# Performance work log

Hardware: AMD Instinct MI355X
Metric: run time of the kernel (lower is better)

Reference implementation:

```python
import jax, jax.numpy as jnp
import numpy as np

N_NODES = 50000
N_EDGES = 800000
SD = 128
N_GRAPHS = 128
HL = 4
VOCAB = 1340
N_CLASSES = 41
BN_EPS = 1e-5


def setup_inputs() -> dict:
    key = jax.random.key(0)
    ks = jax.random.split(key, 20)
    s = 1.0 / np.sqrt(SD)
    inp = {
        "node_ids": jax.random.randint(ks[0], (N_NODES,), 0, VOCAB),
        "edge_index": jax.random.randint(ks[1], (2, N_EDGES), 0, N_NODES),
        "batch": jnp.sort(jax.random.randint(ks[2], (N_NODES,), 0, N_GRAPHS)),
        "emb": jax.random.normal(ks[3], (VOCAB, SD)) * 0.05,
        "in_W1": jax.random.normal(ks[4], (SD, SD)) * s,
        "in_b1": jnp.zeros((SD,)),
        "in_W2": jax.random.normal(ks[5], (SD, SD)) * s,
        "in_b2": jnp.zeros((SD,)),
        "bn_gamma": jnp.ones((SD,)),
        "bn_beta": jnp.zeros((SD,)),
        "bn_mean": jnp.zeros((SD,)),
        "bn_var": jnp.ones((SD,)),
        "out_W1": jax.random.normal(ks[6], (SD, SD)) * s,
        "out_b1": jnp.zeros((SD,)),
        "out_W2": jax.random.normal(ks[7], (SD, SD)) * s,
        "out_b2": jnp.zeros((SD,)),
        "fc1_W": jax.random.normal(ks[8], (SD, SD)) * s,
        "fc1_b": jnp.zeros((SD,)),
        "fc2_W": jax.random.normal(ks[9], (N_CLASSES, SD)) * s,
        "fc2_b": jnp.zeros((N_CLASSES,)),
    }
    return inp


def reference(node_ids, edge_index, batch, emb, in_W1, in_b1, in_W2, in_b2,
              bn_gamma, bn_beta, bn_mean, bn_var,
              out_W1, out_b1, out_W2, out_b2, fc1_W, fc1_b, fc2_W, fc2_b):
    src, dst = edge_index[0], edge_index[1]

    def gin(x, W1, b1, W2, b2):
        # GINConv with eps=0: mlp(x + sum_{j in N(i)} x_j)
        agg = jax.ops.segment_sum(x[src], dst, num_segments=N_NODES)
        h = x + agg
        h = jnp.maximum(h @ W1.T + b1, 0.0)
        return h @ W2.T + b2

    def bn(x):
        # eval-mode BatchNorm1d with running stats
        return (x - bn_mean) * (bn_gamma / jnp.sqrt(bn_var + BN_EPS)) + bn_beta

    x = emb[node_ids]  # [N, SD]
    x = bn(jnp.maximum(gin(x, in_W1, in_b1, in_W2, in_b2), 0.0))
    for _ in range(HL):  # shared weights, repeated hl times
        x = bn(jnp.maximum(gin(x, in_W1, in_b1, in_W2, in_b2), 0.0))
    x = jnp.maximum(gin(x, out_W1, out_b1, out_W2, out_b2), 0.0)
    pooled = jax.ops.segment_sum(x, batch, num_segments=N_GRAPHS)  # [G, SD]
    h = jnp.maximum(pooled @ fc1_W.T + fc1_b, 0.0)
    return h @ fc2_W.T + fc2_b  # [G, 41]
```

## Files before the change

kernel.cpp:

```cpp
#include <hip/hip_runtime.h>

#define NN 50000
#define NE 800000
#define NG 128
#define NC 41
#define CAP 64
#define XG 8
#define RNG 6250

typedef __attribute__((ext_vector_type(8))) short bfrag8;
typedef __attribute__((ext_vector_type(4))) float facc4;

__device__ __forceinline__ float bf2f(unsigned short u) {
  union { unsigned int i; float f; } v; v.i = ((unsigned int)u) << 16; return v.f;
}
__device__ __forceinline__ unsigned short f2bf(float f) {
  union { float f; unsigned int i; } v; v.f = f;
  unsigned int x = v.i;
  x += 0x7fffu + ((x >> 16) & 1u);
  return (unsigned short)(x >> 16);
}
__device__ __forceinline__ void acc_u4(const uint4 u, float* a) {
  union { unsigned int i; float f; } c;
  c.i = u.x << 16;          a[0] += c.f;
  c.i = u.x & 0xffff0000u;  a[1] += c.f;
  c.i = u.y << 16;          a[2] += c.f;
  c.i = u.y & 0xffff0000u;  a[3] += c.f;
  c.i = u.z << 16;          a[4] += c.f;
  c.i = u.z & 0xffff0000u;  a[5] += c.f;
  c.i = u.w << 16;          a[6] += c.f;
  c.i = u.w & 0xffff0000u;  a[7] += c.f;
}
__device__ __forceinline__ unsigned int pack2(float lo, float hi) {
  return (unsigned int)f2bf(lo) | ((unsigned int)f2bf(hi) << 16);
}

__global__ void prep_kernel(const float* __restrict__ W1, const float* __restrict__ W2,
                            const float* __restrict__ oW1, const float* __restrict__ oW2,
                            const float* __restrict__ gamma, const float* __restrict__ beta,
                            const float* __restrict__ mean, const float* __restrict__ var,
                            unsigned short* W1b, unsigned short* W2b,
                            unsigned short* oW1b, unsigned short* oW2b,
                            float* scale, float* shift) {
  int i = blockIdx.x * 256 + threadIdx.x;
  if (i < 128 * 128) {
    W1b[i] = f2bf(W1[i]);
    W2b[i] = f2bf(W2[i]);
    oW1b[i] = f2bf(oW1[i]);
    oW2b[i] = f2bf(oW2[i]);
  }
  if (i < 128) {
    float s = gamma[i] * rsqrtf(var[i] + 1e-5f);
    scale[i] = s;
    shift[i] = beta[i] - mean[i] * s;
  }
}

__global__ void embed_kernel(const int* __restrict__ node_ids, const float* __restrict__ emb,
                             unsigned short* __restrict__ xb) {
  int idx = blockIdx.x * 256 + threadIdx.x;
  if (idx >= NN * 32) return;
  int node = idx >> 5, f = (idx & 31) * 4;
  const float4 v = *(const float4*)&emb[node_ids[node] * 128 + f];
  ushort4 o;
  o.x = f2bf(v.x); o.y = f2bf(v.y); o.z = f2bf(v.z); o.w = f2bf(v.w);
  *(ushort4*)&xb[node * 128 + f] = o;
}

__global__ __launch_bounds__(256) void fill_kernel(const int* __restrict__ ei,
                                                   int* __restrict__ cnt,
                                                   unsigned short* __restrict__ srclist) {
  int b = blockIdx.x;
  int g = b & 7;
  int s = b >> 3;
  int e = s * 256 + threadIdx.x;
  if (e >= NE) return;
  int d = ei[NE + e];
  unsigned int lo = g * RNG;
  if ((unsigned int)(d - lo) < (unsigned int)RNG) {
    int src = ei[e];
    int pos = atomicAdd(&cnt[d], 1);
    if (pos < CAP) srclist[d * CAP + pos] = (unsigned short)src;
  }
}

__global__ __launch_bounds__(256) void agg_kernel(const unsigned short* __restrict__ xb,
                                                  const int* __restrict__ cnt,
                                                  const unsigned short* __restrict__ srclist,
                                                  unsigned short* __restrict__ hb) {
  int tid = threadIdx.x;
  int node = blockIdx.x * 16 + (tid >> 4);
  if (node >= NN) return;
  int f = (tid & 15) * 8;
  float a[8];
  acc_u4(*(const uint4*)&xb[node * 128 + f],
         (a[0]=0.f, a[1]=0.f, a[2]=0.f, a[3]=0.f, a[4]=0.f, a[5]=0.f, a[6]=0.f, a[7]=0.f, a));
  int deg = cnt[node];
  if (deg > CAP) deg = CAP;
  const unsigned short* lst = &srclist[node * CAP];
  int j = 0;
  for (; j + 8 <= deg; j += 8) {
    uint4 u0 = *(const uint4*)&xb[(int)lst[j] * 128 + f];
    uint4 u1 = *(const uint4*)&xb[(int)lst[j + 1] * 128 + f];
    uint4 u2 = *(const uint4*)&xb[(int)lst[j + 2] * 128 + f];
    uint4 u3 = *(const uint4*)&xb[(int)lst[j + 3] * 128 + f];
    uint4 u4 = *(const uint4*)&xb[(int)lst[j + 4] * 128 + f];
    uint4 u5 = *(const uint4*)&xb[(int)lst[j + 5] * 128 + f];
    uint4 u6 = *(const uint4*)&xb[(int)lst[j + 6] * 128 + f];
    uint4 u7 = *(const uint4*)&xb[(int)lst[j + 7] * 128 + f];
    acc_u4(u0, a); acc_u4(u1, a); acc_u4(u2, a); acc_u4(u3, a);
    acc_u4(u4, a); acc_u4(u5, a); acc_u4(u6, a); acc_u4(u7, a);
  }
  for (; j + 4 <= deg; j += 4) {
    uint4 u0 = *(const uint4*)&xb[(int)lst[j] * 128 + f];
    uint4 u1 = *(const uint4*)&xb[(int)lst[j + 1] * 128 + f];
    uint4 u2 = *(const uint4*)&xb[(int)lst[j + 2] * 128 + f];
    uint4 u3 = *(const uint4*)&xb[(int)lst[j + 3] * 128 + f];
    acc_u4(u0, a); acc_u4(u1, a); acc_u4(u2, a); acc_u4(u3, a);
  }
  for (; j < deg; ++j) {
    uint4 u = *(const uint4*)&xb[(int)lst[j] * 128 + f];
    acc_u4(u, a);
  }
  uint4 o;
  o.x = pack2(a[0], a[1]); o.y = pack2(a[2], a[3]);
  o.z = pack2(a[4], a[5]); o.w = pack2(a[6], a[7]);
  *(uint4*)&hb[node * 128 + f] = o;
}

__global__ __launch_bounds__(256) void mlp_kernel(const unsigned short* __restrict__ A,
                                                  const unsigned short* __restrict__ W1b,
                                                  const unsigned short* __restrict__ W2b,
                                                  const float* __restrict__ bias1,
                                                  const float* __restrict__ bias2,
                                                  const float* __restrict__ scale,
                                                  const float* __restrict__ shift,
                                                  unsigned short* __restrict__ Out,
                                                  int M, int mode) {
  __shared__ unsigned short sW[128 * 128];
  __shared__ unsigned short sA[64 * 128];
  int tid = threadIdx.x;
  int bRow = blockIdx.x * 64;

  const uint4* gw1 = (const uint4*)W1b;
#pragma unroll
  for (int p = 0; p < 8; ++p) {
    int g = p * 256 + tid;
    int r = g >> 4, b = g & 15;
    int ph = (b + r) & 15;
    *(uint4*)&sW[(r * 16 + ph) * 8] = gw1[g];
  }
#pragma unroll
  for (int p = 0; p < 4; ++p) {
    int g = p * 256 + tid;
    int r = g >> 4, b = g & 15;
    int ph = (b + r) & 15;
    int grow = bRow + r;
    uint4 v = {0u, 0u, 0u, 0u};
    if (grow < M) v = *(const uint4*)&A[grow * 128 + b * 8];
    *(uint4*)&sA[(r * 16 + ph) * 8] = v;
  }
  __syncthreads();

  int wave = tid >> 6;
  int lane = tid & 63;
  int l16 = lane & 15;
  int quad = lane >> 4;
  int arow = wave * 16 + l16;

  {
    bfrag8 af[4];
#pragma unroll
    for (int k = 0; k < 4; ++k) {
      int ph = (k * 4 + quad + arow) & 15;
      af[k] = *(const bfrag8*)&sA[(arow * 16 + ph) * 8];
    }
    facc4 acc[8];
#pragma unroll
    for (int t = 0; t < 8; ++t) acc[t] = (facc4){0.f, 0.f, 0.f, 0.f};
#pragma unroll
    for (int k = 0; k < 4; ++k) {
#pragma unroll
      for (int t = 0; t < 8; ++t) {
        int r = t * 16 + l16;
        int ph = (k * 4 + quad + r) & 15;
        bfrag8 bf = *(const bfrag8*)&sW[(r * 16 + ph) * 8];
        acc[t] = __builtin_amdgcn_mfma_f32_16x16x32_bf16(af[k], bf, acc[t], 0, 0, 0);
      }
    }
#pragma unroll
    for (int t = 0; t < 8; ++t) {
      int col = t * 16 + l16;
      float b = bias1[col];
      int cb = col >> 3, ce = col & 7;
#pragma unroll
      for (int i = 0; i < 4; ++i) {
        int row = wave * 16 + quad * 4 + i;
        float v = acc[t][i] + b;
        int ph = (cb + row) & 15;
        sA[(row * 16 + ph) * 8 + ce] = f2bf(v > 0.f ? v : 0.f);
      }
    }
  }
  __syncthreads();

  const uint4* gw2 = (const uint4*)W2b;
#pragma unroll
  for (int p = 0; p < 8; ++p) {
    int g = p * 256 + tid;
    int r = g >> 4, b = g & 15;
    int ph = (b + r) & 15;
    *(uint4*)&sW[(r * 16 + ph) * 8] = gw2[g];
  }
  __syncthreads();

  {
    bfrag8 af[4];
#pragma unroll
    for (int k = 0; k < 4; ++k) {
      int ph = (k * 4 + quad + arow) & 15;
      af[k] = *(const bfrag8*)&sA[(arow * 16 + ph) * 8];
    }
    facc4 acc[8];
#pragma unroll
    for (int t = 0; t < 8; ++t) acc[t] = (facc4){0.f, 0.f, 0.f, 0.f};
#pragma unroll
    for (int k = 0; k < 4; ++k) {
#pragma unroll
      for (int t = 0; t < 8; ++t) {
        int r = t * 16 + l16;
        int ph = (k * 4 + quad + r) & 15;
        bfrag8 bf = *(const bfrag8*)&sW[(r * 16 + ph) * 8];
        acc[t] = __builtin_amdgcn_mfma_f32_16x16x32_bf16(af[k], bf, acc[t], 0, 0, 0);
      }
    }
#pragma unroll
    for (int t = 0; t < 8; ++t) {
      int col = t * 16 + l16;
      float b = bias2[col];
      float sc = 1.f, sh = 0.f;
      if (mode == 1) { sc = scale[col]; sh = shift[col]; }
      int cb = col >> 3, ce = col & 7;
#pragma unroll
      for (int i = 0; i < 4; ++i) {
        int row = wave * 16 + quad * 4 + i;
        float v = acc[t][i] + b;
        v = v > 0.f ? v : 0.f;
        if (mode == 1) v = v * sc + sh;
        int ph = (cb + row) & 15;
        sA[(row * 16 + ph) * 8 + ce] = f2bf(v);
      }
    }
  }
  __syncthreads();

#pragma unroll
  for (int p = 0; p < 4; ++p) {
    int g = p * 256 + tid;
    int r = g >> 4, b = g & 15;
    int ph = (b + r) & 15;
    int grow = bRow + r;
    if (grow < M)
      *(uint4*)&Out[grow * 128 + b * 8] = *(const uint4*)&sA[(r * 16 + ph) * 8];
  }
}

__global__ __launch_bounds__(128) void pool_kernel(const unsigned short* __restrict__ xb,
                                                   const int* __restrict__ batch,
                                                   float* __restrict__ pooled) {
  const int CHUNK = 128;
  int start = blockIdx.x * CHUNK;
  int end = start + CHUNK;
  if (end > NN) end = NN;
  int f = threadIdx.x;
  float acc = 0.f;
  int cur = -1;
  for (int i = start; i < end; ++i) {
    int b = batch[i];
    if (b != cur) {
      if (cur >= 0) atomicAdd(&pooled[cur * 128 + f], acc);
      cur = b;
      acc = 0.f;
    }
    acc += bf2f(xb[i * 128 + f]);
  }
  if (cur >= 0) atomicAdd(&pooled[cur * 128 + f], acc);
}

__global__ __launch_bounds__(128) void fc_kernel(const float* __restrict__ pooled,
                                                 const float* __restrict__ W1,
                                                 const float* __restrict__ b1,
                                                 const float* __restrict__ W2,
                                                 const float* __restrict__ b2,
                                                 float* __restrict__ out) {
  __shared__ float sh1[128];
  __shared__ float sp[128];
  int r = blockIdx.x;
  int c = threadIdx.x;
  sp[c] = pooled[r * 128 + c];
  __syncthreads();
  float acc = 0.f;
  for (int k = 0; k < 128; ++k) acc += sp[k] * W1[c * 128 + k];
  acc += b1[c];
  sh1[c] = acc > 0.f ? acc : 0.f;
  __syncthreads();
  if (c < NC) {
    float o = 0.f;
    for (int k = 0; k < 128; ++k) o += sh1[k] * W2[c * 128 + k];
    out[r * NC + c] = o + b2[c];
  }
}

extern "C" void kernel_launch(void* const* d_in, const int* in_sizes, int n_in,
                              void* d_out, int out_size, void* d_ws, size_t ws_size,
                              hipStream_t stream) {
  const int* node_ids = (const int*)d_in[0];
  const int* edge_index = (const int*)d_in[1];
  const int* batch = (const int*)d_in[2];
  const float* emb = (const float*)d_in[3];
  const float* in_W1 = (const float*)d_in[4];
  const float* in_b1 = (const float*)d_in[5];
  const float* in_W2 = (const float*)d_in[6];
  const float* in_b2 = (const float*)d_in[7];
  const float* bn_gamma = (const float*)d_in[8];
  const float* bn_beta = (const float*)d_in[9];
  const float* bn_mean = (const float*)d_in[10];
  const float* bn_var = (const float*)d_in[11];
  const float* out_W1 = (const float*)d_in[12];
  const float* out_b1 = (const float*)d_in[13];
  const float* out_W2 = (const float*)d_in[14];
  const float* out_b2 = (const float*)d_in[15];
  const float* fc1_W = (const float*)d_in[16];
  const float* fc1_b = (const float*)d_in[17];
  const float* fc2_W = (const float*)d_in[18];
  const float* fc2_b = (const float*)d_in[19];
  float* out = (float*)d_out;

  char* ws = (char*)d_ws;
  size_t off = 0;
  auto alloc = [&](size_t bytes) {
    char* p = ws + off;
    off = (off + bytes + 255) & ~(size_t)255;
    return p;
  };
  unsigned short* xb = (unsigned short*)alloc((size_t)NN * 128 * 2);
  unsigned short* hb = (unsigned short*)alloc((size_t)NN * 128 * 2);
  unsigned short* srclist = (unsigned short*)alloc((size_t)NN * CAP * 2);
  int* cnt = (int*)alloc((size_t)NN * 4);
  unsigned short* W1b = (unsigned short*)alloc(128 * 128 * 2);
  unsigned short* W2b = (unsigned short*)alloc(128 * 128 * 2);
  unsigned short* oW1b = (unsigned short*)alloc(128 * 128 * 2);
  unsigned short* oW2b = (unsigned short*)alloc(128 * 128 * 2);
  float* bnscale = (float*)alloc(128 * 4);
  float* bnshift = (float*)alloc(128 * 4);
  float* pooled = (float*)alloc(NG * 128 * 4);

  hipMemsetAsync(cnt, 0, (size_t)NN * 4, stream);
  hipMemsetAsync(pooled, 0, (size_t)NG * 128 * 4, stream);

  prep_kernel<<<64, 256, 0, stream>>>(in_W1, in_W2, out_W1, out_W2,
                                      bn_gamma, bn_beta, bn_mean, bn_var,
                                      W1b, W2b, oW1b, oW2b, bnscale, bnshift);
  int chunks = (NE + 255) / 256;
  fill_kernel<<<chunks * XG, 256, 0, stream>>>(edge_index, cnt, srclist);
  embed_kernel<<<(NN * 32 + 255) / 256, 256, 0, stream>>>(node_ids, emb, xb);

  int mlp_blocks = (NN + 63) / 64;
  for (int l = 0; l < 6; ++l) {
    const unsigned short* w1 = (l < 5) ? W1b : oW1b;
    const unsigned short* w2 = (l < 5) ? W2b : oW2b;
    const float* b1 = (l < 5) ? in_b1 : out_b1;
    const float* b2 = (l < 5) ? in_b2 : out_b2;
    int mode2 = (l < 5) ? 1 : 0;
    agg_kernel<<<(NN + 15) / 16, 256, 0, stream>>>(xb, cnt, srclist, hb);
    mlp_kernel<<<mlp_blocks, 256, 0, stream>>>(hb, w1, w2, b1, b2, bnscale, bnshift,
                                               xb, NN, mode2);
  }

  pool_kernel<<<(NN + 127) / 128, 128, 0, stream>>>(xb, batch, pooled);
  fc_kernel<<<NG, 128, 0, stream>>>(pooled, fc1_W, fc1_b, fc2_W, fc2_b, out);
}
```

Before: 492.5 us.

## Fuse neighbor aggregation, MLP and final pooling into one per-layer kernel

Each GIN layer's gather-sum now runs inside the MLP kernel and writes straight into the shared-memory A tile, so the intermediate hb round trip through global memory and one launch per layer go away. The output buffers are ping-ponged because the layer reads neighbors of other blocks while writing its own output. On the last layer the kernel pools the tile into per-graph sums from shared memory, which removes the separate pool kernel. In exchange, each block now gathers only 64 nodes with a serial loop of four groups, which lowers memory-level parallelism in the gather. The block also holds about 48KB of LDS, which may limit occupancy.

```diff
diff --git a/kernel.cpp b/kernel.cpp
--- a/kernel.cpp
+++ b/kernel.cpp
@@ -84,59 +84,20 @@
   }
 }
 
-__global__ __launch_bounds__(256) void agg_kernel(const unsigned short* __restrict__ xb,
-                                                  const int* __restrict__ cnt,
-                                                  const unsigned short* __restrict__ srclist,
-                                                  unsigned short* __restrict__ hb) {
-  int tid = threadIdx.x;
-  int node = blockIdx.x * 16 + (tid >> 4);
-  if (node >= NN) return;
-  int f = (tid & 15) * 8;
-  float a[8];
-  acc_u4(*(const uint4*)&xb[node * 128 + f],
-         (a[0]=0.f, a[1]=0.f, a[2]=0.f, a[3]=0.f, a[4]=0.f, a[5]=0.f, a[6]=0.f, a[7]=0.f, a));
-  int deg = cnt[node];
-  if (deg > CAP) deg = CAP;
-  const unsigned short* lst = &srclist[node * CAP];
-  int j = 0;
-  for (; j + 8 <= deg; j += 8) {
-    uint4 u0 = *(const uint4*)&xb[(int)lst[j] * 128 + f];
-    uint4 u1 = *(const uint4*)&xb[(int)lst[j + 1] * 128 + f];
-    uint4 u2 = *(const uint4*)&xb[(int)lst[j + 2] * 128 + f];
-    uint4 u3 = *(const uint4*)&xb[(int)lst[j + 3] * 128 + f];
-    uint4 u4 = *(const uint4*)&xb[(int)lst[j + 4] * 128 + f];
-    uint4 u5 = *(const uint4*)&xb[(int)lst[j + 5] * 128 + f];
-    uint4 u6 = *(const uint4*)&xb[(int)lst[j + 6] * 128 + f];
-    uint4 u7 = *(const uint4*)&xb[(int)lst[j + 7] * 128 + f];
-    acc_u4(u0, a); acc_u4(u1, a); acc_u4(u2, a); acc_u4(u3, a);
-    acc_u4(u4, a); acc_u4(u5, a); acc_u4(u6, a); acc_u4(u7, a);
-  }
-  for (; j + 4 <= deg; j += 4) {
-    uint4 u0 = *(const uint4*)&xb[(int)lst[j] * 128 + f];
-    uint4 u1 = *(const uint4*)&xb[(int)lst[j + 1] * 128 + f];
-    uint4 u2 = *(const uint4*)&xb[(int)lst[j + 2] * 128 + f];
-    uint4 u3 = *(const uint4*)&xb[(int)lst[j + 3] * 128 + f];
-    acc_u4(u0, a); acc_u4(u1, a); acc_u4(u2, a); acc_u4(u3, a);
-  }
-  for (; j < deg; ++j) {
-    uint4 u = *(const uint4*)&xb[(int)lst[j] * 128 + f];
-    acc_u4(u, a);
-  }
-  uint4 o;
-  o.x = pack2(a[0], a[1]); o.y = pack2(a[2], a[3]);
-  o.z = pack2(a[4], a[5]); o.w = pack2(a[6], a[7]);
-  *(uint4*)&hb[node * 128 + f] = o;
-}
-
-__global__ __launch_bounds__(256) void mlp_kernel(const unsigned short* __restrict__ A,
-                                                  const unsigned short* __restrict__ W1b,
-                                                  const unsigned short* __restrict__ W2b,
-                                                  const float* __restrict__ bias1,
-                                                  const float* __restrict__ bias2,
-                                                  const float* __restrict__ scale,
-                                                  const float* __restrict__ shift,
-                                                  unsigned short* __restrict__ Out,
-                                                  int M, int mode) {
+__global__ __launch_bounds__(256) void gin_layer_kernel(
+    const unsigned short* __restrict__ xin,
+    const int* __restrict__ cnt,
+    const unsigned short* __restrict__ srclist,
+    const unsigned short* __restrict__ W1b,
+    const unsigned short* __restrict__ W2b,
+    const float* __restrict__ bias1,
+    const float* __restrict__ bias2,
+    const float* __restrict__ scale,
+    const float* __restrict__ shift,
+    unsigned short* __restrict__ Out,
+    const int* __restrict__ batch,
+    float* __restrict__ pooled,
+    int M, int mode, int doPool) {
   __shared__ unsigned short sW[128 * 128];
   __shared__ unsigned short sA[64 * 128];
   int tid = threadIdx.x;
@@ -150,15 +111,54 @@
     int ph = (b + r) & 15;
     *(uint4*)&sW[(r * 16 + ph) * 8] = gw1[g];
   }
-#pragma unroll
-  for (int p = 0; p < 4; ++p) {
-    int g = p * 256 + tid;
-    int r = g >> 4, b = g & 15;
-    int ph = (b + r) & 15;
-    int grow = bRow + r;
-    uint4 v = {0u, 0u, 0u, 0u};
-    if (grow < M) v = *(const uint4*)&A[grow * 128 + b * 8];
-    *(uint4*)&sA[(r * 16 + ph) * 8] = v;
+
+  {
+    int l16 = tid & 15;
+    int sub = tid >> 4;
+    int f = l16 * 8;
+#pragma unroll 1
+    for (int g = 0; g < 4; ++g) {
+      int r = g * 16 + sub;
+      int node = bRow + r;
+      float a[8];
+      a[0]=0.f; a[1]=0.f; a[2]=0.f; a[3]=0.f;
+      a[4]=0.f; a[5]=0.f; a[6]=0.f; a[7]=0.f;
+      if (node < M) {
+        acc_u4(*(const uint4*)&xin[node * 128 + f], a);
+        int deg = cnt[node];
+        if (deg > CAP) deg = CAP;
+        const unsigned short* lst = &srclist[node * CAP];
+        int j = 0;
+        for (; j + 8 <= deg; j += 8) {
+          uint4 u0 = *(const uint4*)&xin[(int)lst[j] * 128 + f];
+          uint4 u1 = *(const uint4*)&xin[(int)lst[j + 1] * 128 + f];
+          uint4 u2 = *(const uint4*)&xin[(int)lst[j + 2] * 128 + f];
+          uint4 u3 = *(const uint4*)&xin[(int)lst[j + 3] * 128 + f];
+          uint4 u4 = *(const uint4*)&xin[(int)lst[j + 4] * 128 + f];
+          uint4 u5 = *(const uint4*)&xin[(int)lst[j + 5] * 128 + f];
+          uint4 u6 = *(const uint4*)&xin[(int)lst[j + 6] * 128 + f];
+          uint4 u7 = *(const uint4*)&xin[(int)lst[j + 7] * 128 + f];
+          acc_u4(u0, a); acc_u4(u1, a); acc_u4(u2, a); acc_u4(u3, a);
+          acc_u4(u4, a); acc_u4(u5, a); acc_u4(u6, a); acc_u4(u7, a);
+        }
+        for (; j + 4 <= deg; j += 4) {
+          uint4 u0 = *(const uint4*)&xin[(int)lst[j] * 128 + f];
+          uint4 u1 = *(const uint4*)&xin[(int)lst[j + 1] * 128 + f];
+          uint4 u2 = *(const uint4*)&xin[(int)lst[j + 2] * 128 + f];
+          uint4 u3 = *(const uint4*)&xin[(int)lst[j + 3] * 128 + f];
+          acc_u4(u0, a); acc_u4(u1, a); acc_u4(u2, a); acc_u4(u3, a);
+        }
+        for (; j < deg; ++j) {
+          uint4 u = *(const uint4*)&xin[(int)lst[j] * 128 + f];
+          acc_u4(u, a);
+        }
+      }
+      int ph = (l16 + r) & 15;
+      uint4 o;
+      o.x = pack2(a[0], a[1]); o.y = pack2(a[2], a[3]);
+      o.z = pack2(a[4], a[5]); o.w = pack2(a[6], a[7]);
+      *(uint4*)&sA[(r * 16 + ph) * 8] = o;
+    }
   }
   __syncthreads();
 
@@ -254,37 +254,37 @@
   }
   __syncthreads();
 
-#pragma unroll
-  for (int p = 0; p < 4; ++p) {
-    int g = p * 256 + tid;
-    int r = g >> 4, b = g & 15;
-    int ph = (b + r) & 15;
-    int grow = bRow + r;
-    if (grow < M)
-      *(uint4*)&Out[grow * 128 + b * 8] = *(const uint4*)&sA[(r * 16 + ph) * 8];
-  }
-}
-
-__global__ __launch_bounds__(128) void pool_kernel(const unsigned short* __restrict__ xb,
-                                                   const int* __restrict__ batch,
-                                                   float* __restrict__ pooled) {
-  const int CHUNK = 128;
-  int start = blockIdx.x * CHUNK;
-  int end = start + CHUNK;
-  if (end > NN) end = NN;
-  int f = threadIdx.x;
-  float acc = 0.f;
-  int cur = -1;
-  for (int i = start; i < end; ++i) {
-    int b = batch[i];
-    if (b != cur) {
-      if (cur >= 0) atomicAdd(&pooled[cur * 128 + f], acc);
-      cur = b;
-      acc = 0.f;
-    }
-    acc += bf2f(xb[i * 128 + f]);
-  }
-  if (cur >= 0) atomicAdd(&pooled[cur * 128 + f], acc);
+  if (doPool) {
+    if (tid < 128) {
+      int fcol = tid;
+      int cb = fcol >> 3, ce = fcol & 7;
+      float acc = 0.f;
+      int cur = -1;
+      for (int r = 0; r < 64; ++r) {
+        int row = bRow + r;
+        if (row >= M) break;
+        int b = batch[row];
+        if (b != cur) {
+          if (cur >= 0) atomicAdd(&pooled[cur * 128 + fcol], acc);
+          cur = b;
+          acc = 0.f;
+        }
+        int ph = (cb + r) & 15;
+        acc += bf2f(sA[(r * 16 + ph) * 8 + ce]);
+      }
+      if (cur >= 0) atomicAdd(&pooled[cur * 128 + fcol], acc);
+    }
+  } else {
+#pragma unroll
+    for (int p = 0; p < 4; ++p) {
+      int g = p * 256 + tid;
+      int r = g >> 4, b = g & 15;
+      int ph = (b + r) & 15;
+      int grow = bRow + r;
+      if (grow < M)
+        *(uint4*)&Out[grow * 128 + b * 8] = *(const uint4*)&sA[(r * 16 + ph) * 8];
+    }
+  }
 }
 
 __global__ __launch_bounds__(128) void fc_kernel(const float* __restrict__ pooled,
@@ -366,17 +366,22 @@
   embed_kernel<<<(NN * 32 + 255) / 256, 256, 0, stream>>>(node_ids, emb, xb);
 
   int mlp_blocks = (NN + 63) / 64;
+  const unsigned short* cur = xb;
+  unsigned short* nxt = hb;
   for (int l = 0; l < 6; ++l) {
     const unsigned short* w1 = (l < 5) ? W1b : oW1b;
     const unsigned short* w2 = (l < 5) ? W2b : oW2b;
     const float* b1 = (l < 5) ? in_b1 : out_b1;
     const float* b2 = (l < 5) ? in_b2 : out_b2;
     int mode2 = (l < 5) ? 1 : 0;
-    agg_kernel<<<(NN + 15) / 16, 256, 0, stream>>>(xb, cnt, srclist, hb);
-    mlp_kernel<<<mlp_blocks, 256, 0, stream>>>(hb, w1, w2, b1, b2, bnscale, bnshift,
-                                               xb, NN, mode2);
-  }
-
-  pool_kernel<<<(NN + 127) / 128, 128, 0, stream>>>(xb, batch, pooled);
+    int doPool = (l == 5) ? 1 : 0;
+    gin_layer_kernel<<<mlp_blocks, 256, 0, stream>>>(
+        cur, cnt, srclist, w1, w2, b1, b2, bnscale, bnshift,
+        nxt, batch, pooled, NN, mode2, doPool);
+    const unsigned short* t = cur;
+    cur = nxt;
+    nxt = (unsigned short*)t;
+  }
+
   fc_kernel<<<NG, 128, 0, stream>>>(pooled, fc1_W, fc1_b, fc2_W, fc2_b, out);
 }
```

Result: faster. 482.2 us (-2.1%).
